# Kernel optimization log

Hardware: AMD Instinct MI355X
Metric: run time of the kernel (lower is better)

## Reference

```python
import jax, jax.numpy as jnp
import numpy as np
from functools import partial

B = 524288      # batch
CH = 30         # channel_num (input dim)
FEA = 42        # feature dim consumed by all classifiers
HID = 64        # assumed hidden width of the (unshown) Feature MLP
NC = 2          # num_class -> number of conditional-domain experts
ND = 6          # num_domain
ALPHA = 1.0

# Gradient Reversal Layer: identity fwd, -alpha * grad bwd
@partial(jax.custom_vjp, nondiff_argnums=(1,))
def grl(x, alpha):
    return x

def _grl_fwd(x, alpha):
    return x, None

def _grl_bwd(alpha, res, g):
    return (-alpha * g,)

grl.defvjp(_grl_fwd, _grl_bwd)


def setup_inputs() -> dict:
    key = jax.random.key(0)
    ks = jax.random.split(key, 24)
    r = lambda k, shape, s=0.1: (jax.random.normal(k, shape, dtype=jnp.float32) * s)
    inp = {
        "x": jax.random.normal(ks[0], (B, CH), dtype=jnp.float32),
        "y": jax.random.randint(ks[1], (B,), 0, NC, dtype=jnp.int32),
        # Feature MLP (assumed: CH -> HID -> FEA with ReLU)
        "W_f1": r(ks[2], (CH, HID)), "b_f1": jnp.zeros((HID,), jnp.float32),
        "W_f2": r(ks[3], (HID, FEA)), "b_f2": jnp.zeros((FEA,), jnp.float32),
        # TaskClassifier: 42 -> 20 -> NC
        "W_t1": r(ks[4], (FEA, 20)), "b_t1": jnp.zeros((20,), jnp.float32),
        "W_t2": r(ks[5], (20, NC)), "b_t2": jnp.zeros((NC,), jnp.float32),
        # prior domain classifier: 42 -> 20 -> 20 -> ND
        "W_p1": r(ks[6], (FEA, 20)), "b_p1": jnp.zeros((20,), jnp.float32),
        "W_p2": r(ks[7], (20, 20)), "b_p2": jnp.zeros((20,), jnp.float32),
        "W_p3": r(ks[8], (20, ND)), "b_p3": jnp.zeros((ND,), jnp.float32),
        # NC conditional domain experts, stacked: [NC, ...]
        "W_c1": r(ks[9], (NC, FEA, 20)), "b_c1": jnp.zeros((NC, 20), jnp.float32),
        "W_c2": r(ks[10], (NC, 20, 20)), "b_c2": jnp.zeros((NC, 20), jnp.float32),
        "W_c3": r(ks[11], (NC, 20, ND)), "b_c3": jnp.zeros((NC, ND), jnp.float32),
    }
    return inp


def reference(x, y, W_f1, b_f1, W_f2, b_f2, W_t1, b_t1, W_t2, b_t2,
              W_p1, b_p1, W_p2, b_p2, W_p3, b_p3,
              W_c1, b_c1, W_c2, b_c2, W_c3, b_c3):
    # feature extractor
    h = jax.nn.relu(x @ W_f1 + b_f1)
    fea = jax.nn.relu(h @ W_f2 + b_f2)              # [B, 42]
    # task head
    t = jax.nn.relu(fea @ W_t1 + b_t1)
    task_predict = t @ W_t2 + b_t2                   # [B, NC]
    # gradient-reversed feature for domain heads
    fr = grl(fea, ALPHA)
    # prior domain classifier
    p = jax.nn.relu(fr @ W_p1 + b_p1)
    p = jax.nn.relu(p @ W_p2 + b_p2)
    pd_predict = p @ W_p3 + b_p3                     # [B, ND]
    # conditional experts: with NC=2 compute all experts, then route by label
    c = jax.nn.relu(jnp.einsum('bf,cfh->bch', fr, W_c1) + b_c1[None])
    c = jax.nn.relu(jnp.einsum('bch,chk->bck', c, W_c2) + b_c2[None])
    cd_all = jnp.einsum('bck,ckd->bcd', c, W_c3) + b_c3[None]   # [B, NC, ND]
    cd_predicts = jnp.take_along_axis(cd_all, y[:, None, None].astype(jnp.int32), axis=1)[:, 0, :]
    return (task_predict, pd_predict, cd_predicts)
```

## Files before the change

kernel.cpp:

```cpp
#include <hip/hip_runtime.h>
#include <hip/hip_bf16.h>

typedef __bf16 bf8 __attribute__((ext_vector_type(8)));
typedef unsigned short u16x8 __attribute__((ext_vector_type(8)));
typedef float f32x4 __attribute__((ext_vector_type(4)));
typedef float f32x2 __attribute__((ext_vector_type(2)));
typedef unsigned int u32x4 __attribute__((ext_vector_type(4)));

union FragU { u16x8 u; bf8 b; u32x4 q; };
union BiasU { f32x4 f; u32x4 q; };

struct __attribute__((packed, aligned(4))) F4u { float v[4]; };
struct __attribute__((packed, aligned(4))) F2u { float v[2]; };

static __device__ __forceinline__ f32x4 MM(const FragU& a, const FragU& b, f32x4 c) {
  return __builtin_amdgcn_mfma_f32_16x16x32_bf16(a.b, b.b, c, 0, 0, 0);
}

#define NBATCH 524288
#define NCH 4
#define SPB (NCH * 16 * 4)
#define NTIL (NBATCH / SPB)
#define GRID 512
#define ITERS (NTIL / GRID)
#define NFRAG 37
#define NLDSF 14

__global__ __launch_bounds__(64) void cdann_prep(
    const float* __restrict__ gWf1, const float* __restrict__ gbf1,
    const float* __restrict__ gWf2, const float* __restrict__ gbf2,
    const float* __restrict__ gWt1, const float* __restrict__ gbt1,
    const float* __restrict__ gWt2, const float* __restrict__ gbt2,
    const float* __restrict__ gWp1, const float* __restrict__ gbp1,
    const float* __restrict__ gWp2, const float* __restrict__ gbp2,
    const float* __restrict__ gWp3, const float* __restrict__ gbp3,
    const float* __restrict__ gWc1, const float* __restrict__ gbc1,
    const float* __restrict__ gWc2, const float* __restrict__ gbc2,
    const float* __restrict__ gWc3, const float* __restrict__ gbc3,
    u32x4* __restrict__ ws)
{
  const int lane = (int)threadIdx.x & 63;
  const int fid = (int)blockIdx.x;
  const int g = lane >> 4;
  const int c15 = lane & 15;

  auto colF2 = [](int nt, int m) -> int {
    if (nt < 2) return 8 * (m >> 2) + 4 * nt + (m & 3);
    const int gm = m >> 2, r = m & 3;
    if (gm == 0) return 32 + r;
    if (gm == 1) return 36 + r;
    if (gm == 2 && r < 2) return 40 + r;
    return -1;
  };

  if (fid >= 34) {
    const int nt = fid - 34;
    BiasU b;
#pragma unroll
    for (int r = 0; r < 4; ++r) {
      const int col = colF2(nt, g * 4 + r);
      b.f[r] = (col >= 0) ? gbf2[col] : 0.f;
    }
    ws[fid * 64 + lane] = b.q;
    return;
  }

  auto v_f1 = [&](int k, int m, int nt) -> float {
    const int n = 32 * (nt >> 1) + 8 * (m >> 2) + 4 * (nt & 1) + (m & 3);
    if (k < 30) return gWf1[k * 64 + n];
    if (k == 30) return gbf1[n];
    return 0.f;
  };
  auto v_f2 = [&](int k, int m, int nt) -> float {
    const int col = colF2(nt, m);
    return (col >= 0) ? gWf2[k * 42 + col] : 0.f;
  };
  auto ffea = [](int v) -> int {
    if (v < 36) return v;
    if (v == 36) return -2;
    if (v >= 40 && v <= 43) return v - 4;
    if (v == 48 || v == 49) return v - 8;
    return -1;
  };
  auto v_q = [&](int k, int m, int nt) -> float {
    const int i = ffea(k);
    if (i == -1) return 0.f;
    const int gm = m >> 2;
    const int u = 4 * nt + (m & 3);
    const int head = u / 5;
    const int f = 5 * gm + (u % 5);
    if (head == 0) return (i == -2) ? gbt1[f] : gWt1[i * 20 + f];
    if (head == 1) return (i == -2) ? gbp1[f] : gWp1[i * 20 + f];
    if (head == 2) return (i == -2) ? gbc1[f] : gWc1[i * 20 + f];
    return (i == -2) ? gbc1[20 + f] : gWc1[(42 + i) * 20 + f];
  };
  auto v_tp = [&](int k, int m, int nt) -> float {
    const int ks = k >> 5, j = k & 7, gk = (k >> 3) & 3;
    const int gm = m >> 2;
    const int u = 4 * nt + (m & 3);
    const int isP2 = (u < 5);
    const int cp = 5 * gm + u;
    const int isT2 = (!isP2 && gm == 0 && (u == 5 || u == 6));
    const int ct = u - 5;
    if (ks == 0) {
      if (j < 5) { const int i = 5 * gk + j; return isT2 ? gWt2[i * 2 + ct] : 0.f; }
      if (j == 7 && gk == 0) { if (isT2) return gbt2[ct]; if (isP2) return gbp2[cp]; }
      return 0.f;
    } else {
      if (j < 5) { const int i = 5 * gk + j; return isP2 ? gWp2[i * 20 + cp] : 0.f; }
      return 0.f;
    }
  };
  auto v_cc = [&](int k, int m, int nt) -> float {
    const int ks = k >> 5, j = k & 7, gk = (k >> 3) & 3;
    const int gm = m >> 2;
    const int u = 4 * nt + (m & 3);
    const int isE0 = (u < 5);
    const int isE1 = (u >= 5 && u < 10);
    const int c0 = 5 * gm + u;
    const int c1 = 5 * gm + (u - 5);
    if (ks == 0) {
      if (j < 5) { const int i = 5 * gk + j; return isE0 ? gWc2[i * 20 + c0] : 0.f; }
      if (j == 7 && gk == 0) { if (isE0) return gbc2[c0]; if (isE1) return gbc2[20 + c1]; }
      return 0.f;
    } else {
      if (j < 5) { const int i = 5 * gk + j; return isE1 ? gWc2[(20 + i) * 20 + c1] : 0.f; }
      return 0.f;
    }
  };
  auto v_o = [&](int k, int m, int nt) -> float {
    const int ks = k >> 5, j = k & 7, gk = (k >> 3) & 3;
    const int gm = m >> 2, r = m & 3;
    int kind = -1, c = 0;
    if (nt == 0) {
      if (gm == 0) { kind = 0; c = r; }
      else if (gm == 1) { if (r < 2) { kind = 0; c = 4 + r; } else { kind = 1; c = r - 2; } }
      else if (gm == 2) { kind = 1; c = 2 + r; }
      else { kind = 2; c = r; }
    } else {
      if (gm == 0 && r < 2) { kind = 2; c = 4 + r; }
    }
    if (kind < 0) return 0.f;
    if (ks == 0) {
      if (j < 5) { const int i = 5 * gk + j; return (kind == 0) ? gWp3[i * 6 + c] : 0.f; }
      if (j < 7) { const int i = 5 * gk + (j - 5); return (kind == 2) ? gWc3[(20 + i) * 6 + c] : 0.f; }
      if (gk == 0) {
        if (kind == 0) return gbp3[c];
        if (kind == 1) return gbc3[c];
        return gbc3[6 + c];
      }
      return 0.f;
    } else {
      if (j < 5) { const int i = 5 * gk + j; return (kind == 1) ? gWc3[i * 6 + c] : 0.f; }
      const int i = 5 * gk + 2 + (j - 5);
      return (kind == 2) ? gWc3[(20 + i) * 6 + c] : 0.f;
    }
  };

  int ks, nt, which;
  if (fid < 4)       { ks = 0;                nt = fid;            which = 0; }
  else if (fid < 10) { int t = fid - 4;  ks = t / 3; nt = t % 3;   which = 1; }
  else if (fid < 20) { int t = fid - 10; ks = t / 5; nt = t % 5;   which = 2; }
  else if (fid < 24) { int t = fid - 20; ks = t / 2; nt = t % 2;   which = 3; }
  else if (fid < 30) { int t = fid - 24; ks = t / 3; nt = t % 3;   which = 4; }
  else               { int t = fid - 30; ks = t / 2; nt = t % 2;   which = 5; }

  FragU f;
#pragma unroll
  for (int j = 0; j < 8; ++j) {
    const int k = ks * 32 + g * 8 + j;
    float v;
    switch (which) {
      case 0: v = v_f1(k, c15, nt); break;
      case 1: v = v_f2(k, c15, nt); break;
      case 2: v = v_q(k, c15, nt); break;
      case 3: v = v_tp(k, c15, nt); break;
      case 4: v = v_cc(k, c15, nt); break;
      default: v = v_o(k, c15, nt); break;
    }
    f.b[j] = (__bf16)v;
  }
  ws[fid * 64 + lane] = f.q;
}

__global__ __launch_bounds__(256, 2) void cdann_fwd(
    const float* __restrict__ gx, const int* __restrict__ gy,
    const u32x4* __restrict__ ws, float* __restrict__ gout)
{
  __shared__ __align__(16) u32x4 lfr[NLDSF * 64];
  const int tid = (int)threadIdx.x;
  const int lane = tid & 63;
  const int w = tid >> 6;
  const int g = lane >> 4;
  const int c15 = lane & 15;

  for (int i = tid; i < NLDSF * 64; i += 256) lfr[i] = ws[20 * 64 + i];

  FragU wF1[4], wF2[2][3], wQ[2][5];
#pragma unroll
  for (int nt = 0; nt < 4; ++nt) wF1[nt].q = ws[nt * 64 + lane];
#pragma unroll
  for (int ks = 0; ks < 2; ++ks) {
#pragma unroll
    for (int nt = 0; nt < 3; ++nt) wF2[ks][nt].q = ws[(4 + ks * 3 + nt) * 64 + lane];
#pragma unroll
    for (int nt = 0; nt < 5; ++nt) wQ[ks][nt].q = ws[(10 + ks * 5 + nt) * 64 + lane];
  }
  f32x4 bF2[3];
#pragma unroll
  for (int nt = 0; nt < 3; ++nt) {
    BiasU b; b.q = ws[(34 + nt) * 64 + lane];
    bF2[nt] = b.f;
  }

#pragma unroll
  for (int nt = 0; nt < 4; ++nt) asm volatile("" : "+v"(wF1[nt].u));
#pragma unroll
  for (int ks = 0; ks < 2; ++ks) {
#pragma unroll
    for (int nt = 0; nt < 3; ++nt) asm volatile("" : "+v"(wF2[ks][nt].u));
#pragma unroll
    for (int nt = 0; nt < 5; ++nt) asm volatile("" : "+v"(wQ[ks][nt].u));
  }
#pragma unroll
  for (int nt = 0; nt < 3; ++nt) asm volatile("" : "+v"(bF2[nt]));

  __syncthreads();

  auto LTP = [&](int ks, int nt) { FragU t; t.q = lfr[(ks * 2 + nt) * 64 + lane]; return t; };
  auto LCC = [&](int ks, int nt) { FragU t; t.q = lfr[(4 + ks * 3 + nt) * 64 + lane]; return t; };
  auto LO  = [&](int ks, int nt) { FragU t; t.q = lfr[(10 + ks * 2 + nt) * 64 + lane]; return t; };

  const f32x4 zf = {0.f, 0.f, 0.f, 0.f};
  const __bf16 one = (__bf16)1.0f;
  const __bf16 zero = (__bf16)0.0f;
  float* const outT = gout;
  float* const outP = gout + (size_t)2 * NBATCH;
  float* const outC = gout + (size_t)8 * NBATCH;

  FragU bxp[NCH];
  int ys[NCH];
  auto loadx = [&](int it) {
    const int base = it * SPB + w * (NCH * 16) + c15;
#pragma unroll
    for (int c = 0; c < NCH; ++c) {
      const int s = base + c * 16;
      const float* xp = gx + (size_t)s * 30 + g * 8;
      float t[8];
      if (g < 3) {
        F4u a0 = *(const F4u*)xp; F4u a1 = *(const F4u*)(xp + 4);
#pragma unroll
        for (int j = 0; j < 4; ++j) { t[j] = a0.v[j]; t[4 + j] = a1.v[j]; }
      } else {
        F4u a0 = *(const F4u*)xp; F2u a1 = *(const F2u*)(xp + 4);
#pragma unroll
        for (int j = 0; j < 4; ++j) t[j] = a0.v[j];
        t[4] = a1.v[0]; t[5] = a1.v[1];
        t[6] = 1.0f; t[7] = 0.0f;
      }
#pragma unroll
      for (int j = 0; j < 8; ++j) bxp[c].b[j] = (__bf16)t[j];
      ys[c] = gy[s];
    }
  };

  loadx((int)blockIdx.x);

  for (int ii = 0; ii < ITERS; ++ii) {
    const int it = (int)blockIdx.x + ii * GRID;
    const int base = it * SPB + w * (NCH * 16) + c15;

    FragU bx[NCH];
    int ysl[NCH];
#pragma unroll
    for (int c = 0; c < NCH; ++c) { bx[c] = bxp[c]; ysl[c] = ys[c]; }

    if (ii + 1 < ITERS) loadx(it + GRID);

    FragU bh0[NCH], bh1[NCH];
#pragma unroll
    for (int c = 0; c < NCH; ++c) {
      f32x4 aH[4];
#pragma unroll
      for (int nt = 0; nt < 4; ++nt) aH[nt] = MM(wF1[nt], bx[c], zf);
#pragma unroll
      for (int j = 0; j < 8; ++j) {
        bh0[c].b[j] = (__bf16)fmaxf(aH[j >> 2][j & 3], 0.f);
        bh1[c].b[j] = (__bf16)fmaxf(aH[2 + (j >> 2)][j & 3], 0.f);
      }
    }

    FragU bf0[NCH], bf1[NCH];
#pragma unroll
    for (int c = 0; c < NCH; ++c) {
      f32x4 aF[3];
#pragma unroll
      for (int nt = 0; nt < 3; ++nt) aF[nt] = MM(wF2[1][nt], bh1[c], MM(wF2[0][nt], bh0[c], zf));
#pragma unroll
      for (int j = 0; j < 8; ++j)
        bf0[c].b[j] = (__bf16)fmaxf(aF[j >> 2][j & 3] + bF2[j >> 2][j & 3], 0.f);
#pragma unroll
      for (int j = 0; j < 4; ++j)
        bf1[c].b[j] = (__bf16)fmaxf(aF[2][j] + bF2[2][j], 0.f);
      bf1[c].b[4] = (g == 0) ? one : zero;
      bf1[c].b[5] = zero; bf1[c].b[6] = zero; bf1[c].b[7] = zero;
    }

#pragma unroll
    for (int p = 0; p < 2; ++p) {
      FragU tp0[2], tp1[2], cc0[2], cc1[2];
#pragma unroll
      for (int ci = 0; ci < 2; ++ci) {
        const int c = 2 * p + ci;
        f32x4 aQ[5];
#pragma unroll
        for (int nt = 0; nt < 5; ++nt) aQ[nt] = MM(wQ[1][nt], bf1[c], MM(wQ[0][nt], bf0[c], zf));
        auto rq = [&](int u) { return (__bf16)fmaxf(aQ[u >> 2][u & 3], 0.f); };
#pragma unroll
        for (int j = 0; j < 5; ++j) {
          tp0[ci].b[j] = rq(j);
          tp1[ci].b[j] = rq(5 + j);
          cc0[ci].b[j] = rq(10 + j);
          cc1[ci].b[j] = rq(15 + j);
        }
        tp0[ci].b[5] = zero; tp0[ci].b[6] = zero; tp0[ci].b[7] = (g == 0) ? one : zero;
        tp1[ci].b[5] = zero; tp1[ci].b[6] = zero; tp1[ci].b[7] = zero;
        cc0[ci].b[5] = zero; cc0[ci].b[6] = zero; cc0[ci].b[7] = (g == 0) ? one : zero;
        cc1[ci].b[5] = zero; cc1[ci].b[6] = zero; cc1[ci].b[7] = zero;
      }
      f32x4 aT[2][2];
#pragma unroll
      for (int nt = 0; nt < 2; ++nt) {
        FragU t0 = LTP(0, nt), t1 = LTP(1, nt);
#pragma unroll
        for (int ci = 0; ci < 2; ++ci)
          aT[ci][nt] = MM(t1, tp1[ci], MM(t0, tp0[ci], zf));
      }
      f32x4 aC[2][3];
#pragma unroll
      for (int nt = 0; nt < 3; ++nt) {
        FragU t0 = LCC(0, nt), t1 = LCC(1, nt);
#pragma unroll
        for (int ci = 0; ci < 2; ++ci)
          aC[ci][nt] = MM(t1, cc1[ci], MM(t0, cc0[ci], zf));
      }
      FragU f50[2], f51[2];
      f32x2 t2v[2];
#pragma unroll
      for (int ci = 0; ci < 2; ++ci) {
#pragma unroll
        for (int j = 0; j < 4; ++j) {
          f50[ci].b[j] = (__bf16)fmaxf(aT[ci][0][j], 0.f);
          f51[ci].b[j] = (__bf16)fmaxf(aC[ci][0][j], 0.f);
        }
        f50[ci].b[4] = (__bf16)fmaxf(aT[ci][1][0], 0.f);
        f50[ci].b[5] = (__bf16)fmaxf(aC[ci][1][1], 0.f);
        f50[ci].b[6] = (__bf16)fmaxf(aC[ci][1][2], 0.f);
        f50[ci].b[7] = (g == 0) ? one : zero;
        f51[ci].b[4] = (__bf16)fmaxf(aC[ci][1][0], 0.f);
        f51[ci].b[5] = (__bf16)fmaxf(aC[ci][1][3], 0.f);
        f51[ci].b[6] = (__bf16)fmaxf(aC[ci][2][0], 0.f);
        f51[ci].b[7] = (__bf16)fmaxf(aC[ci][2][1], 0.f);
        t2v[ci][0] = aT[ci][1][1]; t2v[ci][1] = aT[ci][1][2];
      }
      f32x4 aO0[2], aO1[2];
      {
        FragU o0 = LO(0, 0), o1 = LO(1, 0);
#pragma unroll
        for (int ci = 0; ci < 2; ++ci)
          aO0[ci] = MM(o1, f51[ci], MM(o0, f50[ci], zf));
      }
      {
        FragU o0 = LO(0, 1), o1 = LO(1, 1);
#pragma unroll
        for (int ci = 0; ci < 2; ++ci)
          aO1[ci] = MM(o1, f51[ci], MM(o0, f50[ci], zf));
      }
#pragma unroll
      for (int ci = 0; ci < 2; ++ci) {
        const int c = 2 * p + ci;
        const int s = base + c * 16;
        const int y = ysl[c];
        const f32x4 aO0v = aO0[ci], aO1v = aO1[ci];
        if (g == 0) {
          *(f32x2*)(outT + (size_t)s * 2) = t2v[ci];
          f32x2 pa = {aO0v[0], aO0v[1]}, pb = {aO0v[2], aO0v[3]};
          *(f32x2*)(outP + (size_t)s * 6) = pa;
          *(f32x2*)(outP + (size_t)s * 6 + 2) = pb;
          if (y) { f32x2 cv = {aO1v[0], aO1v[1]}; *(f32x2*)(outC + (size_t)s * 6 + 4) = cv; }
        } else if (g == 1) {
          f32x2 pc = {aO0v[0], aO0v[1]};
          *(f32x2*)(outP + (size_t)s * 6 + 4) = pc;
          if (!y) { f32x2 cv = {aO0v[2], aO0v[3]}; *(f32x2*)(outC + (size_t)s * 6) = cv; }
        } else if (g == 2) {
          if (!y) {
            f32x2 ca = {aO0v[0], aO0v[1]}, cb = {aO0v[2], aO0v[3]};
            *(f32x2*)(outC + (size_t)s * 6 + 2) = ca;
            *(f32x2*)(outC + (size_t)s * 6 + 4) = cb;
          }
        } else {
          if (y) {
            f32x2 ca = {aO0v[0], aO0v[1]}, cb = {aO0v[2], aO0v[3]};
            *(f32x2*)(outC + (size_t)s * 6) = ca;
            *(f32x2*)(outC + (size_t)s * 6 + 2) = cb;
          }
        }
      }
    }
  }
}

extern "C" void kernel_launch(void* const* d_in, const int* in_sizes, int n_in,
                              void* d_out, int out_size, void* d_ws, size_t ws_size,
                              hipStream_t stream) {
  (void)in_sizes; (void)n_in; (void)ws_size; (void)out_size;
  const float* gx  = (const float*)d_in[0];
  const int*   gy  = (const int*)d_in[1];
  const float* Wf1 = (const float*)d_in[2];  const float* bf1 = (const float*)d_in[3];
  const float* Wf2 = (const float*)d_in[4];  const float* bf2 = (const float*)d_in[5];
  const float* Wt1 = (const float*)d_in[6];  const float* bt1 = (const float*)d_in[7];
  const float* Wt2 = (const float*)d_in[8];  const float* bt2 = (const float*)d_in[9];
  const float* Wp1 = (const float*)d_in[10]; const float* bp1 = (const float*)d_in[11];
  const float* Wp2 = (const float*)d_in[12]; const float* bp2 = (const float*)d_in[13];
  const float* Wp3 = (const float*)d_in[14]; const float* bp3 = (const float*)d_in[15];
  const float* Wc1 = (const float*)d_in[16]; const float* bc1 = (const float*)d_in[17];
  const float* Wc2 = (const float*)d_in[18]; const float* bc2 = (const float*)d_in[19];
  const float* Wc3 = (const float*)d_in[20]; const float* bc3 = (const float*)d_in[21];
  float* out = (float*)d_out;
  u32x4* ws = (u32x4*)d_ws;

  cdann_prep<<<dim3(NFRAG), dim3(64), 0, stream>>>(
      Wf1, bf1, Wf2, bf2, Wt1, bt1, Wt2, bt2,
      Wp1, bp1, Wp2, bp2, Wp3, bp3, Wc1, bc1, Wc2, bc2, Wc3, bc3, ws);

  cdann_fwd<<<dim3(GRID), dim3(256), 0, stream>>>(gx, gy, ws, out);
}
```

Measured before the change: 42.22 us.

## Move all weight fragments to LDS and halve per-wave tile to raise occupancy

Weight fragments that were previously held in VGPRs (F1, F2, Q layers and F2 bias) now live in shared memory with the rest, and are reloaded from LDS on each use. The per-wave batch chunk count drops from four 16-row tiles to two, the grid doubles, and launch bounds request four blocks per CU instead of two. The aim is lower register pressure, higher occupancy, and better latency hiding of the global x loads. In exchange, every MFMA operand now comes from LDS, which adds LDS bandwidth and latency and gives less reuse of each fragment load per batch tile.

```diff
diff --git a/kernel.cpp b/kernel.cpp
--- a/kernel.cpp
+++ b/kernel.cpp
@@ -18,13 +18,12 @@
 }
 
 #define NBATCH 524288
-#define NCH 4
+#define NCH 2
 #define SPB (NCH * 16 * 4)
 #define NTIL (NBATCH / SPB)
-#define GRID 512
+#define GRID 1024
 #define ITERS (NTIL / GRID)
 #define NFRAG 37
-#define NLDSF 14
 
 __global__ __launch_bounds__(64) void cdann_prep(
     const float* __restrict__ gWf1, const float* __restrict__ gbf1,
@@ -183,53 +182,21 @@
   ws[fid * 64 + lane] = f.q;
 }
 
-__global__ __launch_bounds__(256, 2) void cdann_fwd(
+__global__ __launch_bounds__(256, 4) void cdann_fwd(
     const float* __restrict__ gx, const int* __restrict__ gy,
     const u32x4* __restrict__ ws, float* __restrict__ gout)
 {
-  __shared__ __align__(16) u32x4 lfr[NLDSF * 64];
+  __shared__ __align__(16) u32x4 lfr[NFRAG * 64];
   const int tid = (int)threadIdx.x;
   const int lane = tid & 63;
   const int w = tid >> 6;
   const int g = lane >> 4;
   const int c15 = lane & 15;
 
-  for (int i = tid; i < NLDSF * 64; i += 256) lfr[i] = ws[20 * 64 + i];
-
-  FragU wF1[4], wF2[2][3], wQ[2][5];
-#pragma unroll
-  for (int nt = 0; nt < 4; ++nt) wF1[nt].q = ws[nt * 64 + lane];
-#pragma unroll
-  for (int ks = 0; ks < 2; ++ks) {
-#pragma unroll
-    for (int nt = 0; nt < 3; ++nt) wF2[ks][nt].q = ws[(4 + ks * 3 + nt) * 64 + lane];
-#pragma unroll
-    for (int nt = 0; nt < 5; ++nt) wQ[ks][nt].q = ws[(10 + ks * 5 + nt) * 64 + lane];
-  }
-  f32x4 bF2[3];
-#pragma unroll
-  for (int nt = 0; nt < 3; ++nt) {
-    BiasU b; b.q = ws[(34 + nt) * 64 + lane];
-    bF2[nt] = b.f;
-  }
-
-#pragma unroll
-  for (int nt = 0; nt < 4; ++nt) asm volatile("" : "+v"(wF1[nt].u));
-#pragma unroll
-  for (int ks = 0; ks < 2; ++ks) {
-#pragma unroll
-    for (int nt = 0; nt < 3; ++nt) asm volatile("" : "+v"(wF2[ks][nt].u));
-#pragma unroll
-    for (int nt = 0; nt < 5; ++nt) asm volatile("" : "+v"(wQ[ks][nt].u));
-  }
-#pragma unroll
-  for (int nt = 0; nt < 3; ++nt) asm volatile("" : "+v"(bF2[nt]));
-
+  for (int i = tid; i < NFRAG * 64; i += 256) lfr[i] = ws[i];
   __syncthreads();
 
-  auto LTP = [&](int ks, int nt) { FragU t; t.q = lfr[(ks * 2 + nt) * 64 + lane]; return t; };
-  auto LCC = [&](int ks, int nt) { FragU t; t.q = lfr[(4 + ks * 3 + nt) * 64 + lane]; return t; };
-  auto LO  = [&](int ks, int nt) { FragU t; t.q = lfr[(10 + ks * 2 + nt) * 64 + lane]; return t; };
+  auto LF = [&](int fid) { FragU t; t.q = lfr[fid * 64 + lane]; return t; };
 
   const f32x4 zf = {0.f, 0.f, 0.f, 0.f};
   const __bf16 one = (__bf16)1.0f;
@@ -270,140 +237,161 @@
     const int it = (int)blockIdx.x + ii * GRID;
     const int base = it * SPB + w * (NCH * 16) + c15;
 
-    FragU bx[NCH];
-    int ysl[NCH];
-#pragma unroll
-    for (int c = 0; c < NCH; ++c) { bx[c] = bxp[c]; ysl[c] = ys[c]; }
+    FragU bxA = bxp[0], bxB = bxp[1];
+    const int yA = ys[0], yB = ys[1];
 
     if (ii + 1 < ITERS) loadx(it + GRID);
 
-    FragU bh0[NCH], bh1[NCH];
-#pragma unroll
-    for (int c = 0; c < NCH; ++c) {
-      f32x4 aH[4];
-#pragma unroll
-      for (int nt = 0; nt < 4; ++nt) aH[nt] = MM(wF1[nt], bx[c], zf);
+    f32x4 aHA[4], aHB[4];
+#pragma unroll
+    for (int nt = 0; nt < 4; ++nt) {
+      FragU t = LF(nt);
+      aHA[nt] = MM(t, bxA, zf);
+      aHB[nt] = MM(t, bxB, zf);
+    }
+    FragU bhA0, bhA1, bhB0, bhB1;
+#pragma unroll
+    for (int j = 0; j < 8; ++j) {
+      bhA0.b[j] = (__bf16)fmaxf(aHA[j >> 2][j & 3], 0.f);
+      bhA1.b[j] = (__bf16)fmaxf(aHA[2 + (j >> 2)][j & 3], 0.f);
+      bhB0.b[j] = (__bf16)fmaxf(aHB[j >> 2][j & 3], 0.f);
+      bhB1.b[j] = (__bf16)fmaxf(aHB[2 + (j >> 2)][j & 3], 0.f);
+    }
+
+    f32x4 aFA[3], aFB[3];
+#pragma unroll
+    for (int nt = 0; nt < 3; ++nt) {
+      FragU t0 = LF(4 + nt), t1 = LF(7 + nt);
+      aFA[nt] = MM(t1, bhA1, MM(t0, bhA0, zf));
+      aFB[nt] = MM(t1, bhB1, MM(t0, bhB0, zf));
+    }
+    FragU bf0[2], bf1[2];
+    {
+      BiasU b0, b1, b2;
+      b0.q = lfr[34 * 64 + lane]; b1.q = lfr[35 * 64 + lane]; b2.q = lfr[36 * 64 + lane];
 #pragma unroll
       for (int j = 0; j < 8; ++j) {
-        bh0[c].b[j] = (__bf16)fmaxf(aH[j >> 2][j & 3], 0.f);
-        bh1[c].b[j] = (__bf16)fmaxf(aH[2 + (j >> 2)][j & 3], 0.f);
-      }
-    }
-
-    FragU bf0[NCH], bf1[NCH];
-#pragma unroll
-    for (int c = 0; c < NCH; ++c) {
-      f32x4 aF[3];
-#pragma unroll
-      for (int nt = 0; nt < 3; ++nt) aF[nt] = MM(wF2[1][nt], bh1[c], MM(wF2[0][nt], bh0[c], zf));
-#pragma unroll
-      for (int j = 0; j < 8; ++j)
-        bf0[c].b[j] = (__bf16)fmaxf(aF[j >> 2][j & 3] + bF2[j >> 2][j & 3], 0.f);
-#pragma unroll
-      for (int j = 0; j < 4; ++j)
-        bf1[c].b[j] = (__bf16)fmaxf(aF[2][j] + bF2[2][j], 0.f);
-      bf1[c].b[4] = (g == 0) ? one : zero;
-      bf1[c].b[5] = zero; bf1[c].b[6] = zero; bf1[c].b[7] = zero;
-    }
-
-#pragma unroll
-    for (int p = 0; p < 2; ++p) {
-      FragU tp0[2], tp1[2], cc0[2], cc1[2];
+        const float bb = (j >> 2) ? b1.f[j & 3] : b0.f[j & 3];
+        bf0[0].b[j] = (__bf16)fmaxf(aFA[j >> 2][j & 3] + bb, 0.f);
+        bf0[1].b[j] = (__bf16)fmaxf(aFB[j >> 2][j & 3] + bb, 0.f);
+      }
+#pragma unroll
+      for (int j = 0; j < 4; ++j) {
+        bf1[0].b[j] = (__bf16)fmaxf(aFA[2][j] + b2.f[j], 0.f);
+        bf1[1].b[j] = (__bf16)fmaxf(aFB[2][j] + b2.f[j], 0.f);
+      }
+      const __bf16 c1v = (g == 0) ? one : zero;
+      bf1[0].b[4] = c1v; bf1[0].b[5] = zero; bf1[0].b[6] = zero; bf1[0].b[7] = zero;
+      bf1[1].b[4] = c1v; bf1[1].b[5] = zero; bf1[1].b[6] = zero; bf1[1].b[7] = zero;
+    }
+
+    f32x4 aQA[5], aQB[5];
+#pragma unroll
+    for (int nt = 0; nt < 5; ++nt) {
+      FragU t0 = LF(10 + nt), t1 = LF(15 + nt);
+      aQA[nt] = MM(t1, bf1[0], MM(t0, bf0[0], zf));
+      aQB[nt] = MM(t1, bf1[1], MM(t0, bf0[1], zf));
+    }
+    FragU tp0[2], tp1[2], cc0[2], cc1[2];
+    {
+      const __bf16 c1v = (g == 0) ? one : zero;
+#pragma unroll
+      for (int j = 0; j < 5; ++j) {
+        tp0[0].b[j] = (__bf16)fmaxf(aQA[j >> 2][j & 3], 0.f);
+        tp1[0].b[j] = (__bf16)fmaxf(aQA[(5 + j) >> 2][(5 + j) & 3], 0.f);
+        cc0[0].b[j] = (__bf16)fmaxf(aQA[(10 + j) >> 2][(10 + j) & 3], 0.f);
+        cc1[0].b[j] = (__bf16)fmaxf(aQA[(15 + j) >> 2][(15 + j) & 3], 0.f);
+        tp0[1].b[j] = (__bf16)fmaxf(aQB[j >> 2][j & 3], 0.f);
+        tp1[1].b[j] = (__bf16)fmaxf(aQB[(5 + j) >> 2][(5 + j) & 3], 0.f);
+        cc0[1].b[j] = (__bf16)fmaxf(aQB[(10 + j) >> 2][(10 + j) & 3], 0.f);
+        cc1[1].b[j] = (__bf16)fmaxf(aQB[(15 + j) >> 2][(15 + j) & 3], 0.f);
+      }
 #pragma unroll
       for (int ci = 0; ci < 2; ++ci) {
-        const int c = 2 * p + ci;
-        f32x4 aQ[5];
-#pragma unroll
-        for (int nt = 0; nt < 5; ++nt) aQ[nt] = MM(wQ[1][nt], bf1[c], MM(wQ[0][nt], bf0[c], zf));
-        auto rq = [&](int u) { return (__bf16)fmaxf(aQ[u >> 2][u & 3], 0.f); };
-#pragma unroll
-        for (int j = 0; j < 5; ++j) {
-          tp0[ci].b[j] = rq(j);
-          tp1[ci].b[j] = rq(5 + j);
-          cc0[ci].b[j] = rq(10 + j);
-          cc1[ci].b[j] = rq(15 + j);
+        tp0[ci].b[5] = zero; tp0[ci].b[6] = zero; tp0[ci].b[7] = c1v;
+        tp1[ci].b[5] = zero; tp1[ci].b[6] = zero; tp1[ci].b[7] = zero;
+        cc0[ci].b[5] = zero; cc0[ci].b[6] = zero; cc0[ci].b[7] = c1v;
+        cc1[ci].b[5] = zero; cc1[ci].b[6] = zero; cc1[ci].b[7] = zero;
+      }
+    }
+
+    f32x4 aT[2][2];
+#pragma unroll
+    for (int nt = 0; nt < 2; ++nt) {
+      FragU t0 = LF(20 + nt), t1 = LF(22 + nt);
+#pragma unroll
+      for (int ci = 0; ci < 2; ++ci)
+        aT[ci][nt] = MM(t1, tp1[ci], MM(t0, tp0[ci], zf));
+    }
+    f32x4 aC[2][3];
+#pragma unroll
+    for (int nt = 0; nt < 3; ++nt) {
+      FragU t0 = LF(24 + nt), t1 = LF(27 + nt);
+#pragma unroll
+      for (int ci = 0; ci < 2; ++ci)
+        aC[ci][nt] = MM(t1, cc1[ci], MM(t0, cc0[ci], zf));
+    }
+
+    FragU f50[2], f51[2];
+    f32x2 t2v[2];
+#pragma unroll
+    for (int ci = 0; ci < 2; ++ci) {
+#pragma unroll
+      for (int j = 0; j < 4; ++j) {
+        f50[ci].b[j] = (__bf16)fmaxf(aT[ci][0][j], 0.f);
+        f51[ci].b[j] = (__bf16)fmaxf(aC[ci][0][j], 0.f);
+      }
+      f50[ci].b[4] = (__bf16)fmaxf(aT[ci][1][0], 0.f);
+      f50[ci].b[5] = (__bf16)fmaxf(aC[ci][1][1], 0.f);
+      f50[ci].b[6] = (__bf16)fmaxf(aC[ci][1][2], 0.f);
+      f50[ci].b[7] = (g == 0) ? one : zero;
+      f51[ci].b[4] = (__bf16)fmaxf(aC[ci][1][0], 0.f);
+      f51[ci].b[5] = (__bf16)fmaxf(aC[ci][1][3], 0.f);
+      f51[ci].b[6] = (__bf16)fmaxf(aC[ci][2][0], 0.f);
+      f51[ci].b[7] = (__bf16)fmaxf(aC[ci][2][1], 0.f);
+      t2v[ci][0] = aT[ci][1][1]; t2v[ci][1] = aT[ci][1][2];
+    }
+
+    f32x4 aO0[2], aO1[2];
+    {
+      FragU o0 = LF(30), o1 = LF(32);
+#pragma unroll
+      for (int ci = 0; ci < 2; ++ci)
+        aO0[ci] = MM(o1, f51[ci], MM(o0, f50[ci], zf));
+    }
+    {
+      FragU o0 = LF(31), o1 = LF(33);
+#pragma unroll
+      for (int ci = 0; ci < 2; ++ci)
+        aO1[ci] = MM(o1, f51[ci], MM(o0, f50[ci], zf));
+    }
+
+#pragma unroll
+    for (int ci = 0; ci < 2; ++ci) {
+      const int s = base + ci * 16;
+      const int y = ci ? yB : yA;
+      const f32x4 aO0v = aO0[ci], aO1v = aO1[ci];
+      if (g == 0) {
+        *(f32x2*)(outT + (size_t)s * 2) = t2v[ci];
+        f32x2 pa = {aO0v[0], aO0v[1]}, pb = {aO0v[2], aO0v[3]};
+        *(f32x2*)(outP + (size_t)s * 6) = pa;
+        *(f32x2*)(outP + (size_t)s * 6 + 2) = pb;
+        if (y) { f32x2 cv = {aO1v[0], aO1v[1]}; *(f32x2*)(outC + (size_t)s * 6 + 4) = cv; }
+      } else if (g == 1) {
+        f32x2 pc = {aO0v[0], aO0v[1]};
+        *(f32x2*)(outP + (size_t)s * 6 + 4) = pc;
+        if (!y) { f32x2 cv = {aO0v[2], aO0v[3]}; *(f32x2*)(outC + (size_t)s * 6) = cv; }
+      } else if (g == 2) {
+        if (!y) {
+          f32x2 ca = {aO0v[0], aO0v[1]}, cb = {aO0v[2], aO0v[3]};
+          *(f32x2*)(outC + (size_t)s * 6 + 2) = ca;
+          *(f32x2*)(outC + (size_t)s * 6 + 4) = cb;
         }
-        tp0[ci].b[5] = zero; tp0[ci].b[6] = zero; tp0[ci].b[7] = (g == 0) ? one : zero;
-        tp1[ci].b[5] = zero; tp1[ci].b[6] = zero; tp1[ci].b[7] = zero;
-        cc0[ci].b[5] = zero; cc0[ci].b[6] = zero; cc0[ci].b[7] = (g == 0) ? one : zero;
-        cc1[ci].b[5] = zero; cc1[ci].b[6] = zero; cc1[ci].b[7] = zero;
-      }
-      f32x4 aT[2][2];
-#pragma unroll
-      for (int nt = 0; nt < 2; ++nt) {
-        FragU t0 = LTP(0, nt), t1 = LTP(1, nt);
-#pragma unroll
-        for (int ci = 0; ci < 2; ++ci)
-          aT[ci][nt] = MM(t1, tp1[ci], MM(t0, tp0[ci], zf));
-      }
-      f32x4 aC[2][3];
-#pragma unroll
-      for (int nt = 0; nt < 3; ++nt) {
-        FragU t0 = LCC(0, nt), t1 = LCC(1, nt);
-#pragma unroll
-        for (int ci = 0; ci < 2; ++ci)
-          aC[ci][nt] = MM(t1, cc1[ci], MM(t0, cc0[ci], zf));
-      }
-      FragU f50[2], f51[2];
-      f32x2 t2v[2];
-#pragma unroll
-      for (int ci = 0; ci < 2; ++ci) {
-#pragma unroll
-        for (int j = 0; j < 4; ++j) {
-          f50[ci].b[j] = (__bf16)fmaxf(aT[ci][0][j], 0.f);
-          f51[ci].b[j] = (__bf16)fmaxf(aC[ci][0][j], 0.f);
-        }
-        f50[ci].b[4] = (__bf16)fmaxf(aT[ci][1][0], 0.f);
-        f50[ci].b[5] = (__bf16)fmaxf(aC[ci][1][1], 0.f);
-        f50[ci].b[6] = (__bf16)fmaxf(aC[ci][1][2], 0.f);
-        f50[ci].b[7] = (g == 0) ? one : zero;
-        f51[ci].b[4] = (__bf16)fmaxf(aC[ci][1][0], 0.f);
-        f51[ci].b[5] = (__bf16)fmaxf(aC[ci][1][3], 0.f);
-        f51[ci].b[6] = (__bf16)fmaxf(aC[ci][2][0], 0.f);
-        f51[ci].b[7] = (__bf16)fmaxf(aC[ci][2][1], 0.f);
-        t2v[ci][0] = aT[ci][1][1]; t2v[ci][1] = aT[ci][1][2];
-      }
-      f32x4 aO0[2], aO1[2];
-      {
-        FragU o0 = LO(0, 0), o1 = LO(1, 0);
-#pragma unroll
-        for (int ci = 0; ci < 2; ++ci)
-          aO0[ci] = MM(o1, f51[ci], MM(o0, f50[ci], zf));
-      }
-      {
-        FragU o0 = LO(0, 1), o1 = LO(1, 1);
-#pragma unroll
-        for (int ci = 0; ci < 2; ++ci)
-          aO1[ci] = MM(o1, f51[ci], MM(o0, f50[ci], zf));
-      }
-#pragma unroll
-      for (int ci = 0; ci < 2; ++ci) {
-        const int c = 2 * p + ci;
-        const int s = base + c * 16;
-        const int y = ysl[c];
-        const f32x4 aO0v = aO0[ci], aO1v = aO1[ci];
-        if (g == 0) {
-          *(f32x2*)(outT + (size_t)s * 2) = t2v[ci];
-          f32x2 pa = {aO0v[0], aO0v[1]}, pb = {aO0v[2], aO0v[3]};
-          *(f32x2*)(outP + (size_t)s * 6) = pa;
-          *(f32x2*)(outP + (size_t)s * 6 + 2) = pb;
-          if (y) { f32x2 cv = {aO1v[0], aO1v[1]}; *(f32x2*)(outC + (size_t)s * 6 + 4) = cv; }
-        } else if (g == 1) {
-          f32x2 pc = {aO0v[0], aO0v[1]};
-          *(f32x2*)(outP + (size_t)s * 6 + 4) = pc;
-          if (!y) { f32x2 cv = {aO0v[2], aO0v[3]}; *(f32x2*)(outC + (size_t)s * 6) = cv; }
-        } else if (g == 2) {
-          if (!y) {
-            f32x2 ca = {aO0v[0], aO0v[1]}, cb = {aO0v[2], aO0v[3]};
-            *(f32x2*)(outC + (size_t)s * 6 + 2) = ca;
-            *(f32x2*)(outC + (size_t)s * 6 + 4) = cb;
-          }
-        } else {
-          if (y) {
-            f32x2 ca = {aO0v[0], aO0v[1]}, cb = {aO0v[2], aO0v[3]};
-            *(f32x2*)(outC + (size_t)s * 6) = ca;
-            *(f32x2*)(outC + (size_t)s * 6 + 2) = cb;
-          }
+      } else {
+        if (y) {
+          f32x2 ca = {aO0v[0], aO0v[1]}, cb = {aO0v[2], aO0v[3]};
+          *(f32x2*)(outC + (size_t)s * 6) = ca;
+          *(f32x2*)(outC + (size_t)s * 6 + 2) = cb;
         }
       }
     }
```

After: 112.6 us. 167% more time.
